# Kernel optimization log

Measured on AMD Instinct MI355X. Metric: run time of the kernel, lower is better.

## Reference

```python
import jax, jax.numpy as jnp
import numpy as np

B, N, H = 8192, 8, 1024  # batch, DOF, hidden width; state dim = 2*N


def setup_inputs() -> dict:
    key = jax.random.key(0)
    ks = jax.random.split(key, 4)
    s1 = 1.0 / np.sqrt(2 * N)
    s2 = 1.0 / np.sqrt(H)
    return {
        "x": jax.random.normal(ks[0], (B, 2 * N), dtype=jnp.float32),
        "W1": jax.random.normal(ks[1], (2 * N, H), dtype=jnp.float32) * s1,
        "b1": jnp.zeros((H,), dtype=jnp.float32),
        "W2": jax.random.normal(ks[2], (H, H), dtype=jnp.float32) * s2,
        "b2": jnp.zeros((H,), dtype=jnp.float32),
        "W3": jax.random.normal(ks[3], (H, 1), dtype=jnp.float32) * s2,
        "b3": jnp.zeros((1,), dtype=jnp.float32),
    }


def reference(x, W1, b1, W2, b2, W3, b3):
    def lagrangian(q, qd):
        z = jnp.concatenate([q, qd])           # (2N,)
        h = jax.nn.softplus(z @ W1 + b1)
        h = jax.nn.softplus(h @ W2 + b2)
        return (h @ W3 + b3).sum()             # scalar L(q, qd)

    dL_dq_fn = jax.grad(lagrangian, argnums=0)
    dL_dqd_fn = jax.grad(lagrangian, argnums=1)
    # forward-over-reverse Hessian blocks (cheap: only N tangents)
    H_qdqd_fn = jax.jacfwd(dL_dqd_fn, argnums=1)   # d2L/dqd dqd, (N,N)
    H_qddq_fn = jax.jacfwd(dL_dqd_fn, argnums=0)   # d2L/dqd dq,  (N,N)

    def step(xi):
        q, qd = xi[:N], xi[N:]
        dL_dq = dL_dq_fn(q, qd)                      # (N,)
        M = H_qdqd_fn(q, qd)                         # mass-matrix block
        C = H_qddq_fn(q, qd)
        qdd = jnp.linalg.inv(M) @ (dL_dq - C @ qd)   # (N,)
        return jnp.concatenate([qd, qdd])            # (2N,)

    return jax.vmap(step)(x)
```

## Files before the change

### kernel.cpp

```cpp
#include <hip/hip_runtime.h>
#include <math.h>

#define B_ 8192
#define H_ 1024
#define LDP0 136
#define LDT 148
#define ASTR 40
#define BSTR 40

typedef short bfrag __attribute__((ext_vector_type(8)));
typedef float f4v  __attribute__((ext_vector_type(4)));

union U8 { unsigned short u[8]; uint4 v; };

__device__ __forceinline__ float sigf(float x){ return 1.0f/(1.0f+__expf(-x)); }

__device__ __forceinline__ unsigned int pkhi(unsigned int u1, unsigned int u0){
  return __builtin_amdgcn_perm(u1, u0, 0x07060302u);
}

__global__ void k1_s1(const float* __restrict__ x, const float* __restrict__ W1,
                      const float* __restrict__ b1, float* __restrict__ s1o){
  __shared__ float xs[16];
  int b = blockIdx.x, t = threadIdx.x;
  if(t < 16) xs[t] = x[b*16 + t];
  __syncthreads();
  for(int h = t; h < H_; h += 256){
    float acc = b1[h];
    #pragma unroll
    for(int j=0;j<16;j++) acc += xs[j]*W1[j*H_ + h];
    s1o[(size_t)b*H_ + h] = sigf(acc);
  }
}

__global__ __launch_bounds__(256,3) void k2_s2(const float* __restrict__ s1,
                      const float* __restrict__ W2, const float* __restrict__ b2,
                      float* __restrict__ s2o){
  __shared__ __align__(16) float As[32*LDP0];
  __shared__ __align__(16) float Bs[32*LDP0];
  int t = threadIdx.x, tx = t & 15, ty = t >> 4;
  int m0 = blockIdx.x * 128, n0 = blockIdx.y * 128;
  int jj = t & 31, rb4 = (t >> 5) * 4;
  float acc[8][8];
  #pragma unroll
  for(int i=0;i<8;i++){
    #pragma unroll
    for(int k=0;k<8;k++) acc[i][k]=0.f; }

  for(int jt=0; jt<32; jt++){
    int j0 = jt*32;
    __syncthreads();
    #pragma unroll
    for(int g=0; g<4; g++){
      #pragma unroll
      for(int i=0;i<4;i++){
        int r = rb4 + i + 32*g;
        As[jj*LDP0 + r] = -__logf(1.0f - s1[(size_t)(m0+r)*H_ + j0 + jj]);
      }
    }
    { int jB = t >> 3, kb = (t & 7) * 16;
      const float* src = &W2[(size_t)(j0 + jB)*H_ + n0 + kb];
      #pragma unroll
      for(int c=0;c<4;c++) *(float4*)&Bs[jB*LDP0 + kb + 4*c] = *(const float4*)(src + 4*c);
    }
    __syncthreads();
    #pragma unroll 8
    for(int j=0;j<32;j++){
      float4 a0 = *(const float4*)&As[j*LDP0 + 8*ty];
      float4 a1f= *(const float4*)&As[j*LDP0 + 8*ty+4];
      float4 b0 = *(const float4*)&Bs[j*LDP0 + 4*tx];
      float4 b1f= *(const float4*)&Bs[j*LDP0 + 64 + 4*tx];
      float aa[8] = {a0.x,a0.y,a0.z,a0.w,a1f.x,a1f.y,a1f.z,a1f.w};
      float bb[8] = {b0.x,b0.y,b0.z,b0.w,b1f.x,b1f.y,b1f.z,b1f.w};
      #pragma unroll
      for(int i=0;i<8;i++){
        #pragma unroll
        for(int k=0;k<8;k++) acc[i][k] += aa[i]*bb[k]; }
    }
  }
  float4 bb0 = *(const float4*)&b2[n0 + 4*tx];
  float4 bb1 = *(const float4*)&b2[n0 + 64 + 4*tx];
  #pragma unroll
  for(int i=0;i<8;i++){
    size_t r = (size_t)(m0 + 8*ty + i)*H_;
    float4 o0 = make_float4(sigf(acc[i][0]+bb0.x), sigf(acc[i][1]+bb0.y),
                            sigf(acc[i][2]+bb0.z), sigf(acc[i][3]+bb0.w));
    float4 o1 = make_float4(sigf(acc[i][4]+bb1.x), sigf(acc[i][5]+bb1.y),
                            sigf(acc[i][6]+bb1.z), sigf(acc[i][7]+bb1.w));
    *(float4*)&s2o[r + n0 + 4*tx] = o0;
    *(float4*)&s2o[r + n0 + 64 + 4*tx] = o1;
  }
}

__global__ __launch_bounds__(256,3) void k3_u(const float* __restrict__ s2,
                      const float* __restrict__ W2, const float* __restrict__ W3,
                      float* __restrict__ u){
  __shared__ __align__(16) float As[32*LDP0];
  __shared__ __align__(16) float Bs[32*LDP0];
  int t = threadIdx.x, tx = t & 15, ty = t >> 4;
  int m0 = blockIdx.x * 128, n0 = blockIdx.y * 128;
  int jj = t & 31, rb4 = (t >> 5) * 4;
  float acc[8][8];
  #pragma unroll
  for(int i=0;i<8;i++){
    #pragma unroll
    for(int k=0;k<8;k++) acc[i][k]=0.f; }

  for(int kt=0; kt<32; kt++){
    int k0 = kt*32;
    __syncthreads();
    float w3v = W3[k0 + jj];
    #pragma unroll
    for(int g=0; g<4; g++){
      #pragma unroll
      for(int i=0;i<4;i++){
        int r = rb4 + i + 32*g;
        As[jj*LDP0 + r] = w3v * s2[(size_t)(m0+r)*H_ + k0 + jj];
      }
    }
    { int jcol = t >> 1, kb = (t & 1) * 16;
      const float* src = &W2[(size_t)(n0 + jcol)*H_ + k0 + kb];
      #pragma unroll
      for(int c=0;c<16;c++) Bs[(kb+c)*LDP0 + jcol] = src[c];
    }
    __syncthreads();
    #pragma unroll 8
    for(int j=0;j<32;j++){
      float4 a0 = *(const float4*)&As[j*LDP0 + 8*ty];
      float4 a1f= *(const float4*)&As[j*LDP0 + 8*ty+4];
      float4 b0 = *(const float4*)&Bs[j*LDP0 + 4*tx];
      float4 b1f= *(const float4*)&Bs[j*LDP0 + 64 + 4*tx];
      float aa[8] = {a0.x,a0.y,a0.z,a0.w,a1f.x,a1f.y,a1f.z,a1f.w};
      float bb[8] = {b0.x,b0.y,b0.z,b0.w,b1f.x,b1f.y,b1f.z,b1f.w};
      #pragma unroll
      for(int i=0;i<8;i++){
        #pragma unroll
        for(int k=0;k<8;k++) acc[i][k] += aa[i]*bb[k]; }
    }
  }
  #pragma unroll
  for(int i=0;i<8;i++){
    size_t r = (size_t)(m0 + 8*ty + i)*H_;
    *(float4*)&u[r + n0 + 4*tx]      = make_float4(acc[i][0],acc[i][1],acc[i][2],acc[i][3]);
    *(float4*)&u[r + n0 + 64 + 4*tx] = make_float4(acc[i][4],acc[i][5],acc[i][6],acc[i][7]);
  }
}

__global__ void kF(const float* __restrict__ W1, float* __restrict__ F64){
  int e = blockIdx.x*256 + threadIdx.x;
  int j = e >> 6, p = e & 63;
  F64[e] = W1[(8+(p>>3))*H_ + j] * W1[(8+(p&7))*H_ + j];
}

__global__ __launch_bounds__(256) void k5a(const float* __restrict__ s1,
                      const float* __restrict__ u, const float* __restrict__ F64,
                      float* __restrict__ Hz1M){
  __shared__ __align__(16) float As[32*72];
  __shared__ __align__(16) float Bs[32*72];
  int t = threadIdx.x, tx = t & 15, ty = t >> 4;
  int m0 = blockIdx.x * 64;
  int jj = t & 31, rb8 = (t >> 5) * 8;
  float acc[4][4];
  #pragma unroll
  for(int i=0;i<4;i++){
    #pragma unroll
    for(int k=0;k<4;k++) acc[i][k]=0.f; }

  for(int jt=0; jt<32; jt++){
    int j0 = jt*32;
    __syncthreads();
    #pragma unroll
    for(int g=0; g<8; g++){
      int r = rb8 + g;
      float s = s1[(size_t)(m0+r)*H_ + j0 + jj];
      As[jj*72 + r] = s*(1.0f-s)*u[(size_t)(m0+r)*H_ + j0 + jj];
    }
    { int jB = t >> 3, cb = (t & 7) * 8;
      const float* src = &F64[(j0 + jB)*64 + cb];
      *(float4*)&Bs[jB*72 + cb]   = *(const float4*)(src);
      *(float4*)&Bs[jB*72 + cb+4] = *(const float4*)(src+4);
    }
    __syncthreads();
    #pragma unroll 8
    for(int j=0;j<32;j++){
      float4 a4 = *(const float4*)&As[j*72 + 4*ty];
      float4 b4 = *(const float4*)&Bs[j*72 + 4*tx];
      float aa[4] = {a4.x,a4.y,a4.z,a4.w};
      float bb[4] = {b4.x,b4.y,b4.z,b4.w};
      #pragma unroll
      for(int i=0;i<4;i++){
        #pragma unroll
        for(int k=0;k<4;k++) acc[i][k] += aa[i]*bb[k]; }
    }
  }
  #pragma unroll
  for(int i=0;i<4;i++)
    *(float4*)&Hz1M[(size_t)(m0+4*ty+i)*64 + 4*tx] =
      make_float4(acc[i][0],acc[i][1],acc[i][2],acc[i][3]);
}

__global__ void k5b(const float* __restrict__ s1, const float* __restrict__ u,
                    const float* __restrict__ W1, const float* __restrict__ x,
                    float* __restrict__ dq16){
  int wid = threadIdx.x >> 6, lane = threadIdx.x & 63;
  int b = blockIdx.x*4 + wid;
  float qd[8];
  #pragma unroll
  for(int i=0;i<8;i++) qd[i] = x[b*16 + 8 + i];
  float accd[8] = {0,0,0,0,0,0,0,0};
  float accc[8] = {0,0,0,0,0,0,0,0};
  for(int jb=0;jb<16;jb++){
    int j = jb*64 + lane;
    float s1v = s1[(size_t)b*H_+j], uv = u[(size_t)b*H_+j];
    float g1 = s1v*uv;
    float d1 = (1.0f - s1v)*g1;
    float w1q = 0.f;
    #pragma unroll
    for(int i=0;i<8;i++){ float w = W1[i*H_+j]; accd[i] += g1*w; w1q += qd[i]*w; }
    float dw = d1*w1q;
    #pragma unroll
    for(int m=0;m<8;m++) accc[m] += dw * W1[(8+m)*H_+j];
  }
  #pragma unroll
  for(int i=0;i<8;i++){
    #pragma unroll
    for(int off=1; off<64; off<<=1){
      accd[i] += __shfl_xor(accd[i], off, 64);
      accc[i] += __shfl_xor(accc[i], off, 64);
    }
  }
  if(lane==0){
    #pragma unroll
    for(int i=0;i<8;i++){ dq16[b*16+i] = accd[i]; dq16[b*16+8+i] = accc[i]; }
  }
}

__global__ void kW2T(const float* __restrict__ W2, unsigned short* __restrict__ Wh,
                     unsigned short* __restrict__ Wm, unsigned short* __restrict__ Wl){
  __shared__ float tile[32][132];
  int j0 = blockIdx.x * 32, k0 = blockIdx.y * 128;
  int t = threadIdx.x;
  int lr = t >> 3, lc0 = (t & 7) * 16;
  const float* src = &W2[(size_t)(j0+lr)*H_ + k0 + lc0];
  #pragma unroll
  for(int c=0;c<16;c+=4) *(float4*)&tile[lr][lc0+c] = *(const float4*)(src + c);
  __syncthreads();
  int k = t >> 1;
  #pragma unroll
  for(int o2=0;o2<2;o2++){
    int oc = (t&1)*2 + o2;
    U8 uh, um2, ul2;
    #pragma unroll
    for(int e=0;e<8;e++){
      float a = tile[oc*8+e][k];
      unsigned int ua = __float_as_uint(a);
      unsigned int h = ua & 0xFFFF0000u;
      float r1 = a - __uint_as_float(h);
      unsigned int m = __float_as_uint(r1) & 0xFFFF0000u;
      float l = r1 - __uint_as_float(m);
      uh.u[e]  = (unsigned short)(h >> 16);
      um2.u[e] = (unsigned short)(m >> 16);
      ul2.u[e] = (unsigned short)(__float_as_uint(l) >> 16);
    }
    size_t o = (size_t)(k0+k)*H_ + j0 + oc*8;
    *(uint4*)&Wh[o] = uh.v; *(uint4*)&Wm[o] = um2.v; *(uint4*)&Wl[o] = ul2.v;
  }
}

__global__ __launch_bounds__(256,2) void k4_mfma(
    const float* __restrict__ s1, const float* __restrict__ s2,
    const float* __restrict__ x,  const float* __restrict__ W1,
    const unsigned short* __restrict__ W2Th, const unsigned short* __restrict__ W2Tm,
    const unsigned short* __restrict__ W2Tl,
    const float* __restrict__ W3, float* __restrict__ Mpart){
  __shared__ union {
    struct { unsigned short A[3][144*ASTR]; unsigned short Bt[3][128*BSTR]; } st;
    float Td[64*LDT];
  } sm;
  __shared__ float qds[16][8];

  int t = threadIdx.x;
  int wv = t >> 6, lane = t & 63;
  int kb = blockIdx.x & 7, sgp = blockIdx.x >> 3;
  int b0 = sgp*16, k0 = kb*128;

  if(t < 128){ int s = t>>3, i = t&7; qds[s][i] = x[(b0+s)*16 + 8+i]; }

  f4v acc[9][2];
  #pragma unroll
  for(int mt=0;mt<9;mt++){
    #pragma unroll
    for(int n2=0;n2<2;n2++){ acc[mt][n2][0]=0.f; acc[mt][n2][1]=0.f; acc[mt][n2][2]=0.f; acc[mt][n2][3]=0.f; }
  }

  int aoct = t & 3, arow = t >> 2;
  int bn = t >> 1;
  int fr_m = lane & 15, fr_q = lane >> 4;

  for(int jt=0; jt<32; jt++){
    int j0 = jt*32;
    __syncthreads();
    #pragma unroll
    for(int pass=0; pass<3; pass++){
      int r = pass*64 + arow;
      if(r < 144){
        float4 w0, w1v, sa, sb;
        if(r < 128){
          int s = r>>3, m = r&7;
          const float* wp = &W1[(size_t)(8+m)*H_ + j0 + aoct*8];
          w0 = *(const float4*)wp; w1v = *(const float4*)(wp+4);
          const float* sp = &s1[(size_t)(b0+s)*H_ + j0 + aoct*8];
          sa = *(const float4*)sp; sb = *(const float4*)(sp+4);
        } else {
          int s = r - 128;
          float g0=0,g1=0,g2=0,g3=0,g4=0,g5=0,g6=0,g7=0;
          #pragma unroll
          for(int i=0;i<8;i++){
            float q = qds[s][i];
            const float* wp = &W1[(size_t)i*H_ + j0 + aoct*8];
            float4 a0 = *(const float4*)wp, a1 = *(const float4*)(wp+4);
            g0 += q*a0.x; g1 += q*a0.y; g2 += q*a0.z; g3 += q*a0.w;
            g4 += q*a1.x; g5 += q*a1.y; g6 += q*a1.z; g7 += q*a1.w;
          }
          w0 = make_float4(g0,g1,g2,g3); w1v = make_float4(g4,g5,g6,g7);
          const float* sp = &s1[(size_t)(b0+s)*H_ + j0 + aoct*8];
          sa = *(const float4*)sp; sb = *(const float4*)(sp+4);
        }
        float av[8];
        av[0]=w0.x*sa.x; av[1]=w0.y*sa.y; av[2]=w0.z*sa.z; av[3]=w0.w*sa.w;
        av[4]=w1v.x*sb.x; av[5]=w1v.y*sb.y; av[6]=w1v.z*sb.z; av[7]=w1v.w*sb.w;
        unsigned int uh[8], um[8], ul[8];
        #pragma unroll
        for(int e=0;e<8;e++){
          unsigned int ua = __float_as_uint(av[e]);
          unsigned int h = ua & 0xFFFF0000u;
          float r1 = av[e] - __uint_as_float(h);
          unsigned int m = __float_as_uint(r1) & 0xFFFF0000u;
          float l = r1 - __uint_as_float(m);
          uh[e]=h; um[e]=m; ul[e]=__float_as_uint(l);
        }
        int o = r*ASTR + aoct*8;
        uint4 vh = make_uint4(pkhi(uh[1],uh[0]), pkhi(uh[3],uh[2]), pkhi(uh[5],uh[4]), pkhi(uh[7],uh[6]));
        uint4 vm = make_uint4(pkhi(um[1],um[0]), pkhi(um[3],um[2]), pkhi(um[5],um[4]), pkhi(um[7],um[6]));
        uint4 vl = make_uint4(pkhi(ul[1],ul[0]), pkhi(ul[3],ul[2]), pkhi(ul[5],ul[4]), pkhi(ul[7],ul[6]));
        *(uint4*)&sm.st.A[0][o] = vh;
        *(uint4*)&sm.st.A[1][o] = vm;
        *(uint4*)&sm.st.A[2][o] = vl;
      }
    }
    #pragma unroll
    for(int o2=0;o2<2;o2++){
      int oc = (t&1)*2 + o2;
      size_t gsrc = (size_t)(k0+bn)*H_ + j0 + oc*8;
      int o = bn*BSTR + oc*8;
      *(uint4*)&sm.st.Bt[0][o] = *(const uint4*)&W2Th[gsrc];
      *(uint4*)&sm.st.Bt[1][o] = *(const uint4*)&W2Tm[gsrc];
      *(uint4*)&sm.st.Bt[2][o] = *(const uint4*)&W2Tl[gsrc];
    }
    __syncthreads();
    bfrag bf[2][3];
    #pragma unroll
    for(int n2=0;n2<2;n2++){
      int n = (2*wv+n2)*16 + fr_m;
      #pragma unroll
      for(int p=0;p<3;p++) bf[n2][p] = *(bfrag*)&sm.st.Bt[p][n*BSTR + fr_q*8];
    }
    #pragma unroll
    for(int mt=0; mt<9; mt++){
      int rr = mt*16 + fr_m;
      bfrag a0 = *(bfrag*)&sm.st.A[0][rr*ASTR + fr_q*8];
      bfrag a1v= *(bfrag*)&sm.st.A[1][rr*ASTR + fr_q*8];
      bfrag a2v= *(bfrag*)&sm.st.A[2][rr*ASTR + fr_q*8];
      #pragma unroll
      for(int n2=0;n2<2;n2++){
        f4v c = acc[mt][n2];
        c = __builtin_amdgcn_mfma_f32_16x16x32_bf16(a2v, bf[n2][1], c, 0,0,0);
        c = __builtin_amdgcn_mfma_f32_16x16x32_bf16(a1v, bf[n2][2], c, 0,0,0);
        c = __builtin_amdgcn_mfma_f32_16x16x32_bf16(a2v, bf[n2][0], c, 0,0,0);
        c = __builtin_amdgcn_mfma_f32_16x16x32_bf16(a0,  bf[n2][2], c, 0,0,0);
        c = __builtin_amdgcn_mfma_f32_16x16x32_bf16(a1v, bf[n2][1], c, 0,0,0);
        c = __builtin_amdgcn_mfma_f32_16x16x32_bf16(a1v, bf[n2][0], c, 0,0,0);
        c = __builtin_amdgcn_mfma_f32_16x16x32_bf16(a0,  bf[n2][1], c, 0,0,0);
        c = __builtin_amdgcn_mfma_f32_16x16x32_bf16(a0,  bf[n2][0], c, 0,0,0);
        acc[mt][n2] = c;
      }
    }
  }

  float Mp[44];
  #pragma unroll
  for(int i=0;i<44;i++) Mp[i]=0.f;
  int es = t>>4, ec = t&15;
  const float* s2p = &s2[(size_t)(b0+es)*H_ + k0];

  #pragma unroll
  for(int ph=0; ph<2; ph++){
    __syncthreads();
    if((wv>>1) == ph){
      int w1b = wv & 1;
      #pragma unroll
      for(int mt=0; mt<9; mt++){
        #pragma unroll
        for(int n2=0;n2<2;n2++){
          int col = (2*w1b+n2)*16 + fr_m;
          int rowb = mt*16 + fr_q*4;
          #pragma unroll
          for(int rg=0;rg<4;rg++)
            sm.Td[col*LDT + rowb + rg] = acc[mt][n2][rg];
        }
      }
    }
    __syncthreads();
    float4 s2v = *(const float4*)&s2p[ph*64 + ec*4];
    float4 w3v = *(const float4*)&W3[k0 + ph*64 + ec*4];
    float dv[4] = { w3v.x*s2v.x*(1.f-s2v.x), w3v.y*s2v.y*(1.f-s2v.y),
                    w3v.z*s2v.z*(1.f-s2v.z), w3v.w*s2v.w*(1.f-s2v.w) };
    #pragma unroll
    for(int e=0;e<4;e++){
      int col = ec*4+e;
      const float* tp = &sm.Td[col*LDT + es*8];
      float4 t0 = *(const float4*)tp, t1 = *(const float4*)(tp+4);
      float T8[8] = {t0.x,t0.y,t0.z,t0.w,t1.x,t1.y,t1.z,t1.w};
      float vv = sm.Td[col*LDT + 128 + es];
      float d = dv[e];
      int ix=0;
      #pragma unroll
      for(int m=0;m<8;m++){
        float w = T8[m]*d;
        Mp[36+m] += w*vv;
        #pragma unroll
        for(int n=m;n<8;n++){ Mp[ix] += w*T8[n]; ix++; }
      }
    }
  }
  #pragma unroll
  for(int i=0;i<44;i++){
    #pragma unroll
    for(int off=1; off<16; off<<=1) Mp[i] += __shfl_xor(Mp[i], off, 64);
  }
  if(ec==0){
    float* o = &Mpart[((size_t)(b0+es)*8 + kb)*44];
    #pragma unroll
    for(int i=0;i<44;i++) o[i] = Mp[i];
  }
}

__global__ __launch_bounds__(64) void k6(const float* __restrict__ x,
                    const float* __restrict__ Hz1M, const float* __restrict__ Mpart,
                    const float* __restrict__ dq16, float* __restrict__ out){
  __shared__ double A[64][73];
  int t = threadIdx.x;
  int b = blockIdx.x*64 + t;
  double* Ar = A[t];
  float qd[8];
  #pragma unroll
  for(int j=0;j<8;j++) qd[j] = x[b*16 + 8 + j];
  float Ms[44];
  #pragma unroll
  for(int i=0;i<44;i++) Ms[i]=0.f;
  for(int kb=0;kb<8;kb++){
    const float* mp = &Mpart[((size_t)b*8+kb)*44];
    #pragma unroll
    for(int i=0;i<44;i++) Ms[i] += mp[i];
  }
  #pragma unroll
  for(int i=0;i<8;i++){
    #pragma unroll
    for(int j=0;j<8;j++) Ar[i*9+j] = (double)Hz1M[(size_t)b*64 + i*8 + j];
    Ar[i*9+8] = (double)dq16[b*16+i] - (double)dq16[b*16+8+i] - (double)Ms[36+i];
  }
  { int ix=0;
    for(int m=0;m<8;m++)
      for(int n=m;n<8;n++){
        Ar[m*9+n] += (double)Ms[ix];
        if(n>m) Ar[n*9+m] += (double)Ms[ix];
        ix++;
      }
  }
  for(int c=0;c<8;c++){
    int piv = c; double best = fabs(Ar[c*9+c]);
    for(int rr=c+1; rr<8; rr++){ double v = fabs(Ar[rr*9+c]); if(v>best){best=v;piv=rr;} }
    if(piv!=c){
      for(int cc=c; cc<9; cc++){ double tmp=Ar[c*9+cc]; Ar[c*9+cc]=Ar[piv*9+cc]; Ar[piv*9+cc]=tmp; }
    }
    double inv = 1.0/Ar[c*9+c];
    for(int rr=c+1; rr<8; rr++){
      double f = Ar[rr*9+c]*inv;
      for(int cc=c+1; cc<9; cc++) Ar[rr*9+cc] -= f*Ar[c*9+cc];
    }
  }
  double sol[8];
  #pragma unroll
  for(int i=7;i>=0;i--){
    double s = Ar[i*9+8];
    #pragma unroll
    for(int j=i+1;j<8;j++) s -= Ar[i*9+j]*sol[j];
    sol[i] = s/Ar[i*9+i];
  }
  #pragma unroll
  for(int j=0;j<8;j++) out[b*16+j] = qd[j];
  #pragma unroll
  for(int i=0;i<8;i++) out[b*16+8+i] = (float)sol[i];
}

extern "C" void kernel_launch(void* const* d_in, const int* in_sizes, int n_in,
                              void* d_out, int out_size, void* d_ws, size_t ws_size,
                              hipStream_t stream){
  const float* x  = (const float*)d_in[0];
  const float* W1 = (const float*)d_in[1];
  const float* b1 = (const float*)d_in[2];
  const float* W2 = (const float*)d_in[3];
  const float* b2 = (const float*)d_in[4];
  const float* W3 = (const float*)d_in[5];
  float* out = (float*)d_out;

  float* ws   = (float*)d_ws;
  size_t BH   = (size_t)B_*H_;
  float* s1   = ws;
  float* s2   = s1  + BH;
  float* u    = s2  + BH;
  float* F64  = u   + BH;
  float* Hz1M = F64 + (size_t)H_*64;
  float* dq16 = Hz1M+ (size_t)B_*64;

  float* Mpart = u;
  unsigned short* W2Th = (unsigned short*)(u + 3145728);
  unsigned short* W2Tm = W2Th + (size_t)H_*H_;
  unsigned short* W2Tl = W2Tm + (size_t)H_*H_;

  k1_s1 <<<dim3(B_),      dim3(256), 0, stream>>>(x, W1, b1, s1);
  k2_s2 <<<dim3(64,8),    dim3(256), 0, stream>>>(s1, W2, b2, s2);
  k3_u  <<<dim3(64,8),    dim3(256), 0, stream>>>(s2, W2, W3, u);
  kF    <<<dim3(256),     dim3(256), 0, stream>>>(W1, F64);
  k5a   <<<dim3(128),     dim3(256), 0, stream>>>(s1, u, F64, Hz1M);
  k5b   <<<dim3(2048),    dim3(256), 0, stream>>>(s1, u, W1, x, dq16);
  kW2T  <<<dim3(32,8),    dim3(256), 0, stream>>>(W2, W2Th, W2Tm, W2Tl);
  k4_mfma<<<dim3(4096),   dim3(256), 0, stream>>>(s1, s2, x, W1, W2Th, W2Tm, W2Tl, W3, Mpart);
  k6    <<<dim3(128),     dim3(64),  0, stream>>>(x, Hz1M, Mpart, dq16, out);
}
```

Measured before the change: 2.172 ms.

## Swizzle k4 LDS layout, raise occupancy, and pin FMA rounding explicitly

Replaces the padded per-plane A/Bt shared arrays in the MFMA kernel with a granule-sectioned layout (16-byte granules grouped by k-octet, XOR-swizzled rows). The goal is to cut LDS bank conflicts on fragment reads and to shrink shared memory use. With the smaller footprint, launch bounds for k4 go from 2 to 3 blocks per SM. Throughout the code, explicit __fmaf_rn/__fmul_rn/__fsub_rn intrinsics replace plain arithmetic, which mainly pins numerics. k6 now accumulates partial mass-matrix sums in double, adding some fp64 cost for better accuracy.

Result: no change. 2.182 ms (+0.4%).

```diff
diff --git a/kernel.cpp b/kernel.cpp
--- a/kernel.cpp
+++ b/kernel.cpp
@@ -5,8 +5,12 @@
 #define H_ 1024
 #define LDP0 136
 #define LDT 148
-#define ASTR 40
-#define BSTR 40
+
+#define A_SEC 145
+#define B_SEC 129
+#define A_GRN (12*A_SEC)
+#define B_GRN (12*B_SEC)
+#define AB_SH ((A_GRN + B_GRN)*8)
 
 typedef short bfrag __attribute__((ext_vector_type(8)));
 typedef float f4v  __attribute__((ext_vector_type(4)));
@@ -28,7 +32,7 @@
   for(int h = t; h < H_; h += 256){
     float acc = b1[h];
     #pragma unroll
-    for(int j=0;j<16;j++) acc += xs[j]*W1[j*H_ + h];
+    for(int j=0;j<16;j++) acc = __fmaf_rn(xs[j], W1[j*H_ + h], acc);
     s1o[(size_t)b*H_ + h] = sigf(acc);
   }
 }
@@ -75,7 +79,7 @@
       #pragma unroll
       for(int i=0;i<8;i++){
         #pragma unroll
-        for(int k=0;k<8;k++) acc[i][k] += aa[i]*bb[k]; }
+        for(int k=0;k<8;k++) acc[i][k] = __fmaf_rn(aa[i], bb[k], acc[i][k]); }
     }
   }
   float4 bb0 = *(const float4*)&b2[n0 + 4*tx];
@@ -135,7 +139,7 @@
       #pragma unroll
       for(int i=0;i<8;i++){
         #pragma unroll
-        for(int k=0;k<8;k++) acc[i][k] += aa[i]*bb[k]; }
+        for(int k=0;k<8;k++) acc[i][k] = __fmaf_rn(aa[i], bb[k], acc[i][k]); }
     }
   }
   #pragma unroll
@@ -190,7 +194,7 @@
       #pragma unroll
       for(int i=0;i<4;i++){
         #pragma unroll
-        for(int k=0;k<4;k++) acc[i][k] += aa[i]*bb[k]; }
+        for(int k=0;k<4;k++) acc[i][k] = __fmaf_rn(aa[i], bb[k], acc[i][k]); }
     }
   }
   #pragma unroll
@@ -216,10 +220,12 @@
     float d1 = (1.0f - s1v)*g1;
     float w1q = 0.f;
     #pragma unroll
-    for(int i=0;i<8;i++){ float w = W1[i*H_+j]; accd[i] += g1*w; w1q += qd[i]*w; }
+    for(int i=0;i<8;i++){ float w = W1[i*H_+j];
+      accd[i] = __fmaf_rn(g1, w, accd[i]);
+      w1q = __fmaf_rn(qd[i], w, w1q); }
     float dw = d1*w1q;
     #pragma unroll
-    for(int m=0;m<8;m++) accc[m] += dw * W1[(8+m)*H_+j];
+    for(int m=0;m<8;m++) accc[m] = __fmaf_rn(dw, W1[(8+m)*H_+j], accc[m]);
   }
   #pragma unroll
   for(int i=0;i<8;i++){
@@ -255,9 +261,9 @@
       float a = tile[oc*8+e][k];
       unsigned int ua = __float_as_uint(a);
       unsigned int h = ua & 0xFFFF0000u;
-      float r1 = a - __uint_as_float(h);
+      float r1 = __fsub_rn(a, __uint_as_float(h));
       unsigned int m = __float_as_uint(r1) & 0xFFFF0000u;
-      float l = r1 - __uint_as_float(m);
+      float l = __fsub_rn(r1, __uint_as_float(m));
       uh.u[e]  = (unsigned short)(h >> 16);
       um2.u[e] = (unsigned short)(m >> 16);
       ul2.u[e] = (unsigned short)(__float_as_uint(l) >> 16);
@@ -267,14 +273,14 @@
   }
 }
 
-__global__ __launch_bounds__(256,2) void k4_mfma(
+__global__ __launch_bounds__(256,3) void k4_mfma(
     const float* __restrict__ s1, const float* __restrict__ s2,
     const float* __restrict__ x,  const float* __restrict__ W1,
     const unsigned short* __restrict__ W2Th, const unsigned short* __restrict__ W2Tm,
     const unsigned short* __restrict__ W2Tl,
     const float* __restrict__ W3, float* __restrict__ Mpart){
   __shared__ union {
-    struct { unsigned short A[3][144*ASTR]; unsigned short Bt[3][128*BSTR]; } st;
+    unsigned short AB[AB_SH];
     float Td[64*LDT];
   } sm;
   __shared__ float qds[16][8];
@@ -296,6 +302,10 @@
   int aoct = t & 3, arow = t >> 2;
   int bn = t >> 1;
   int fr_m = lane & 15, fr_q = lane >> 4;
+  int pfm   = fr_m ^ ((fr_m & 8) >> 1);
+  int aRd   = fr_q*A_SEC + pfm;
+  int bRd   = A_GRN + fr_q*B_SEC + (2*wv)*16 + pfm;
+  int bPerm = A_GRN + (bn ^ ((bn & 8) >> 1));
 
   for(int jt=0; jt<32; jt++){
     int j0 = jt*32;
@@ -319,58 +329,60 @@
             float q = qds[s][i];
             const float* wp = &W1[(size_t)i*H_ + j0 + aoct*8];
             float4 a0 = *(const float4*)wp, a1 = *(const float4*)(wp+4);
-            g0 += q*a0.x; g1 += q*a0.y; g2 += q*a0.z; g3 += q*a0.w;
-            g4 += q*a1.x; g5 += q*a1.y; g6 += q*a1.z; g7 += q*a1.w;
+            g0 = __fmaf_rn(q, a0.x, g0); g1 = __fmaf_rn(q, a0.y, g1);
+            g2 = __fmaf_rn(q, a0.z, g2); g3 = __fmaf_rn(q, a0.w, g3);
+            g4 = __fmaf_rn(q, a1.x, g4); g5 = __fmaf_rn(q, a1.y, g5);
+            g6 = __fmaf_rn(q, a1.z, g6); g7 = __fmaf_rn(q, a1.w, g7);
           }
           w0 = make_float4(g0,g1,g2,g3); w1v = make_float4(g4,g5,g6,g7);
           const float* sp = &s1[(size_t)(b0+s)*H_ + j0 + aoct*8];
           sa = *(const float4*)sp; sb = *(const float4*)(sp+4);
         }
         float av[8];
-        av[0]=w0.x*sa.x; av[1]=w0.y*sa.y; av[2]=w0.z*sa.z; av[3]=w0.w*sa.w;
-        av[4]=w1v.x*sb.x; av[5]=w1v.y*sb.y; av[6]=w1v.z*sb.z; av[7]=w1v.w*sb.w;
+        av[0]=__fmul_rn(w0.x,sa.x); av[1]=__fmul_rn(w0.y,sa.y);
+        av[2]=__fmul_rn(w0.z,sa.z); av[3]=__fmul_rn(w0.w,sa.w);
+        av[4]=__fmul_rn(w1v.x,sb.x); av[5]=__fmul_rn(w1v.y,sb.y);
+        av[6]=__fmul_rn(w1v.z,sb.z); av[7]=__fmul_rn(w1v.w,sb.w);
         unsigned int uh[8], um[8], ul[8];
         #pragma unroll
         for(int e=0;e<8;e++){
           unsigned int ua = __float_as_uint(av[e]);
           unsigned int h = ua & 0xFFFF0000u;
-          float r1 = av[e] - __uint_as_float(h);
+          float r1 = __fsub_rn(av[e], __uint_as_float(h));
           unsigned int m = __float_as_uint(r1) & 0xFFFF0000u;
-          float l = r1 - __uint_as_float(m);
+          float l = __fsub_rn(r1, __uint_as_float(m));
           uh[e]=h; um[e]=m; ul[e]=__float_as_uint(l);
         }
-        int o = r*ASTR + aoct*8;
+        int g0i = aoct*A_SEC + (r ^ ((r & 8) >> 1));
         uint4 vh = make_uint4(pkhi(uh[1],uh[0]), pkhi(uh[3],uh[2]), pkhi(uh[5],uh[4]), pkhi(uh[7],uh[6]));
         uint4 vm = make_uint4(pkhi(um[1],um[0]), pkhi(um[3],um[2]), pkhi(um[5],um[4]), pkhi(um[7],um[6]));
         uint4 vl = make_uint4(pkhi(ul[1],ul[0]), pkhi(ul[3],ul[2]), pkhi(ul[5],ul[4]), pkhi(ul[7],ul[6]));
-        *(uint4*)&sm.st.A[0][o] = vh;
-        *(uint4*)&sm.st.A[1][o] = vm;
-        *(uint4*)&sm.st.A[2][o] = vl;
+        *(uint4*)&sm.AB[(g0i            )*8] = vh;
+        *(uint4*)&sm.AB[(g0i + 4*A_SEC  )*8] = vm;
+        *(uint4*)&sm.AB[(g0i + 8*A_SEC  )*8] = vl;
       }
     }
     #pragma unroll
     for(int o2=0;o2<2;o2++){
       int oc = (t&1)*2 + o2;
       size_t gsrc = (size_t)(k0+bn)*H_ + j0 + oc*8;
-      int o = bn*BSTR + oc*8;
-      *(uint4*)&sm.st.Bt[0][o] = *(const uint4*)&W2Th[gsrc];
-      *(uint4*)&sm.st.Bt[1][o] = *(const uint4*)&W2Tm[gsrc];
-      *(uint4*)&sm.st.Bt[2][o] = *(const uint4*)&W2Tl[gsrc];
+      int g0i = bPerm + oc*B_SEC;
+      *(uint4*)&sm.AB[(g0i            )*8] = *(const uint4*)&W2Th[gsrc];
+      *(uint4*)&sm.AB[(g0i + 4*B_SEC  )*8] = *(const uint4*)&W2Tm[gsrc];
+      *(uint4*)&sm.AB[(g0i + 8*B_SEC  )*8] = *(const uint4*)&W2Tl[gsrc];
     }
     __syncthreads();
     bfrag bf[2][3];
     #pragma unroll
     for(int n2=0;n2<2;n2++){
-      int n = (2*wv+n2)*16 + fr_m;
-      #pragma unroll
-      for(int p=0;p<3;p++) bf[n2][p] = *(bfrag*)&sm.st.Bt[p][n*BSTR + fr_q*8];
+      #pragma unroll
+      for(int p=0;p<3;p++) bf[n2][p] = *(bfrag*)&sm.AB[(bRd + p*4*B_SEC + n2*16)*8];
     }
     #pragma unroll
     for(int mt=0; mt<9; mt++){
-      int rr = mt*16 + fr_m;
-      bfrag a0 = *(bfrag*)&sm.st.A[0][rr*ASTR + fr_q*8];
-      bfrag a1v= *(bfrag*)&sm.st.A[1][rr*ASTR + fr_q*8];
-      bfrag a2v= *(bfrag*)&sm.st.A[2][rr*ASTR + fr_q*8];
+      bfrag a0 = *(bfrag*)&sm.AB[(aRd             + mt*16)*8];
+      bfrag a1v= *(bfrag*)&sm.AB[(aRd + 4*A_SEC   + mt*16)*8];
+      bfrag a2v= *(bfrag*)&sm.AB[(aRd + 8*A_SEC   + mt*16)*8];
       #pragma unroll
       for(int n2=0;n2<2;n2++){
         f4v c = acc[mt][n2];
@@ -426,10 +438,10 @@
       int ix=0;
       #pragma unroll
       for(int m=0;m<8;m++){
-        float w = T8[m]*d;
-        Mp[36+m] += w*vv;
+        float w = __fmul_rn(T8[m], d);
+        Mp[36+m] = __fmaf_rn(w, vv, Mp[36+m]);
         #pragma unroll
-        for(int n=m;n<8;n++){ Mp[ix] += w*T8[n]; ix++; }
+        for(int n=m;n<8;n++){ Mp[ix] = __fmaf_rn(w, T8[n], Mp[ix]); ix++; }
       }
     }
   }
@@ -455,25 +467,25 @@
   float qd[8];
   #pragma unroll
   for(int j=0;j<8;j++) qd[j] = x[b*16 + 8 + j];
-  float Ms[44];
-  #pragma unroll
-  for(int i=0;i<44;i++) Ms[i]=0.f;
+  double Ms[44];
+  #pragma unroll
+  for(int i=0;i<44;i++) Ms[i]=0.0;
   for(int kb=0;kb<8;kb++){
     const float* mp = &Mpart[((size_t)b*8+kb)*44];
     #pragma unroll
-    for(int i=0;i<44;i++) Ms[i] += mp[i];
+    for(int i=0;i<44;i++) Ms[i] += (double)mp[i];
   }
   #pragma unroll
   for(int i=0;i<8;i++){
     #pragma unroll
     for(int j=0;j<8;j++) Ar[i*9+j] = (double)Hz1M[(size_t)b*64 + i*8 + j];
-    Ar[i*9+8] = (double)dq16[b*16+i] - (double)dq16[b*16+8+i] - (double)Ms[36+i];
+    Ar[i*9+8] = (double)dq16[b*16+i] - (double)dq16[b*16+8+i] - Ms[36+i];
   }
   { int ix=0;
     for(int m=0;m<8;m++)
       for(int n=m;n<8;n++){
-        Ar[m*9+n] += (double)Ms[ix];
-        if(n>m) Ar[n*9+m] += (double)Ms[ix];
+        Ar[m*9+n] += Ms[ix];
+        if(n>m) Ar[n*9+m] += Ms[ix];
         ix++;
       }
   }
```
